# Kernel tuning notes

Hardware: AMD Instinct MI355X
Metric: run time of the kernel (lower is better)

The kernel has to match this reference:

```python
import jax, jax.numpy as jnp
import numpy as np

N_NODES = 50000
N_EDGES = 300000
F_IN, HID, N_CLS = 256, 256, 128


def _glorot_linear(key, fan_in, fan_out):
    # torch.nn.Linear-style uniform init, kaiming bound 1/sqrt(fan_in)
    s = 1.0 / np.sqrt(fan_in)
    return jax.random.uniform(key, (fan_in, fan_out), jnp.float32, -s, s)


def setup_inputs() -> dict:
    key = jax.random.key(0)
    ks = jax.random.split(key, 8)
    x = jax.random.normal(ks[0], (N_NODES, F_IN), jnp.float32)
    edge_index = jax.random.randint(ks[1], (2, N_EDGES), 0, N_NODES, dtype=jnp.int32)
    return {
        "x": x,
        "edge_index": edge_index,
        "W1": _glorot_linear(ks[2], F_IN, HID), "b1": jnp.zeros((HID,), jnp.float32),
        "W2": _glorot_linear(ks[3], HID, HID),  "b2": jnp.zeros((HID,), jnp.float32),
        "W3": _glorot_linear(ks[4], HID, HID),  "b3": jnp.zeros((HID,), jnp.float32),
        "W4": _glorot_linear(ks[5], HID, N_CLS), "b4": jnp.zeros((N_CLS,), jnp.float32),
    }


def _gcn_conv(x, W, b, src, dst, norm, n):
    # x' = D^{-1/2} (A + I) D^{-1/2} X W + b   (PyG GCNConv default)
    h = x @ W                                  # [N, out]
    msg = h[src] * norm[:, None]               # gather + edge scaling  [E', out]
    return jax.ops.segment_sum(msg, dst, num_segments=n) + b


def reference(x, edge_index, W1, b1, W2, b2, W3, b3, W4, b4):
    n = x.shape[0]
    loops = jnp.arange(n, dtype=edge_index.dtype)
    src = jnp.concatenate([edge_index[0], loops])  # add self-loops
    dst = jnp.concatenate([edge_index[1], loops])
    # symmetric normalization: deg over target nodes (unit edge weights)
    deg = jax.ops.segment_sum(jnp.ones_like(dst, jnp.float32), dst, num_segments=n)
    dis = jnp.where(deg > 0, jax.lax.rsqrt(jnp.maximum(deg, 1.0)), 0.0)
    norm = dis[src] * dis[dst]                     # [E']

    h = jax.nn.relu(_gcn_conv(x, W1, b1, src, dst, norm, n))
    h = jax.nn.relu(_gcn_conv(h, W2, b2, src, dst, norm, n))
    h = jax.nn.relu(_gcn_conv(h, W3, b3, src, dst, norm, n))
    h = _gcn_conv(h, W4, b4, src, dst, norm, n)    # [N, C]

    # global_add_pool with batch == zeros -> single-graph sum pool
    pooled = jnp.sum(h, axis=0, keepdims=True)     # [1, C]
    return (pooled, jax.nn.log_softmax(pooled, axis=1))
```

## Files before the change

### kernel.cpp

```cpp
#include <hip/hip_runtime.h>


typedef __attribute__((ext_vector_type(8))) short short8;
typedef __attribute__((ext_vector_type(4))) short short4v;
typedef __attribute__((ext_vector_type(4))) float float4v;

__device__ __forceinline__ unsigned short f2b(float f) {
    unsigned int u = __builtin_bit_cast(unsigned int, f);
    u += 0x7fffu + ((u >> 16) & 1u);
    return (unsigned short)(u >> 16);
}
__device__ __forceinline__ float b2f(unsigned short b) {
    unsigned int u = ((unsigned int)b) << 16;
    return __builtin_bit_cast(float, u);
}


__global__ void count_kernel(const int* __restrict__ dst, int* __restrict__ cnt, int E) {
    int i = blockIdx.x * blockDim.x + threadIdx.x;
    if (i < E) atomicAdd(&cnt[dst[i]], 1);
}

__global__ void blocksum_kernel(const int* __restrict__ cnt, int* __restrict__ bsum, int N) {
    __shared__ int s[256];
    int t = threadIdx.x;
    int i = blockIdx.x * 256 + t;
    s[t] = (i < N) ? cnt[i] : 0;
    __syncthreads();
    for (int d = 128; d > 0; d >>= 1) {
        if (t < d) s[t] += s[t + d];
        __syncthreads();
    }
    if (t == 0) bsum[blockIdx.x] = s[0];
}

__global__ void bscan_kernel(int* __restrict__ bsum, int B) {
    __shared__ int s[256];
    int t = threadIdx.x;
    int v = (t < B) ? bsum[t] : 0;
    s[t] = v;
    __syncthreads();
    for (int d = 1; d < 256; d <<= 1) {
        int x = (t >= d) ? s[t - d] : 0;
        __syncthreads();
        s[t] += x;
        __syncthreads();
    }
    if (t < B) bsum[t] = s[t] - v;
}

__global__ void finalize_kernel(const int* __restrict__ cnt, const int* __restrict__ bsum,
                                int* __restrict__ offs, int* __restrict__ cursor,
                                float* __restrict__ dis, int N, int E) {
    __shared__ int s[256];
    int t = threadIdx.x;
    int i = blockIdx.x * 256 + t;
    int c = (i < N) ? cnt[i] : 0;
    s[t] = c;
    __syncthreads();
    for (int d = 1; d < 256; d <<= 1) {
        int x = (t >= d) ? s[t - d] : 0;
        __syncthreads();
        s[t] += x;
        __syncthreads();
    }
    if (i < N) {
        int ex = bsum[blockIdx.x] + s[t] - c;
        offs[i] = ex;
        cursor[i] = ex;
        dis[i] = rsqrtf((float)(c + 1));
    }
    if (blockIdx.x == 0 && t == 0) offs[N] = E;
}

__global__ void scatter_kernel(const int* __restrict__ src, const int* __restrict__ dst,
                               const float* __restrict__ dis, int* __restrict__ cursor,
                               int* __restrict__ csr_src, float* __restrict__ csr_nrm, int E) {
    int i = blockIdx.x * blockDim.x + threadIdx.x;
    if (i < E) {
        int s = src[i], d = dst[i];
        int pos = atomicAdd(&cursor[d], 1);
        csr_src[pos] = s;
        csr_nrm[pos] = dis[s] * dis[d];
    }
}

__global__ void outsum_kernel(const int* __restrict__ src, const int* __restrict__ dst,
                              const float* __restrict__ dis, float* __restrict__ t, int E) {
    int i = blockIdx.x * blockDim.x + threadIdx.x;
    if (i < E) atomicAdd(&t[src[i]], dis[dst[i]]);
}


__global__ void convert_x_kernel(const float* __restrict__ x, unsigned short* __restrict__ xb,
                                 int total4) {
    int i = blockIdx.x * blockDim.x + threadIdx.x;
    if (i < total4) {
        float4 v = *(const float4*)&x[i * 4];
        ushort4 o;
        o.x = f2b(v.x); o.y = f2b(v.y); o.z = f2b(v.z); o.w = f2b(v.w);
        *(ushort4*)&xb[i * 4] = o;
    }
}

__global__ void convert_wt_kernel(const float* __restrict__ W1, const float* __restrict__ W2,
                                  const float* __restrict__ W3, unsigned short* __restrict__ Wt1,
                                  unsigned short* __restrict__ Wt2, unsigned short* __restrict__ Wt3) {
    const float* W = (blockIdx.y == 0) ? W1 : (blockIdx.y == 1) ? W2 : W3;
    unsigned short* Wt = (blockIdx.y == 0) ? Wt1 : (blockIdx.y == 1) ? Wt2 : Wt3;
    int n = blockIdx.x;
    int k = threadIdx.x;
    Wt[n * 256 + k] = f2b(W[k * 256 + n]);
}

__global__ __launch_bounds__(256, 2) void gemm_bf16_kernel(
        const unsigned short* __restrict__ A, const unsigned short* __restrict__ Wt,
        unsigned short* __restrict__ C, int M) {
    __shared__ unsigned short As[128 * 72];
    __shared__ unsigned short Bs[128 * 72];
    const int tid = threadIdx.x;
    const int lane = tid & 63;
    const int wave = tid >> 6;
    const int l15 = lane & 15;
    const int quad = lane >> 4;
    const int wm = wave & 1;
    const int wn = wave >> 1;
    const int m0 = blockIdx.x * 128;
    const int n0 = blockIdx.y * 128;

    float4v acc[4][4] = {};

    const int srow = tid >> 3;
    const int skof = (tid & 7) * 8;

    for (int kk = 0; kk < 256; kk += 64) {
#pragma unroll
        for (int p = 0; p < 4; p++) {
            int row = p * 32 + srow;
            int gm = m0 + row;
            float4 av = make_float4(0.f, 0.f, 0.f, 0.f);
            if (gm < M) av = *(const float4*)&A[(size_t)gm * 256 + kk + skof];
            *(float4*)&As[row * 72 + skof] = av;
            float4 bv = *(const float4*)&Wt[(size_t)(n0 + row) * 256 + kk + skof];
            *(float4*)&Bs[row * 72 + skof] = bv;
        }
        __syncthreads();
#pragma unroll
        for (int ks = 0; ks < 64; ks += 32) {
            short8 af[4], bf[4];
#pragma unroll
            for (int mi = 0; mi < 4; mi++)
                af[mi] = *(const short8*)&As[(wm * 64 + mi * 16 + l15) * 72 + ks + quad * 8];
#pragma unroll
            for (int nj = 0; nj < 4; nj++)
                bf[nj] = *(const short8*)&Bs[(wn * 64 + nj * 16 + l15) * 72 + ks + quad * 8];
#pragma unroll
            for (int mi = 0; mi < 4; mi++)
#pragma unroll
                for (int nj = 0; nj < 4; nj++)
                    acc[mi][nj] = __builtin_amdgcn_mfma_f32_16x16x32_bf16(
                        af[mi], bf[nj], acc[mi][nj], 0, 0, 0);
        }
        __syncthreads();
    }

#pragma unroll
    for (int mi = 0; mi < 4; mi++) {
#pragma unroll
        for (int r = 0; r < 4; r++) {
            int row = m0 + wm * 64 + mi * 16 + quad * 4 + r;
            if (row < M) {
#pragma unroll
                for (int nj = 0; nj < 4; nj++) {
                    int col = n0 + wn * 64 + nj * 16 + l15;
                    C[(size_t)row * 256 + col] = f2b(acc[mi][nj][r]);
                }
            }
        }
    }
}

template <int RELU>
__global__ __launch_bounds__(256) void agg_bf16_kernel(
        const unsigned short* __restrict__ T, const float* __restrict__ bias,
        const int* __restrict__ offs, const int* __restrict__ csr_src,
        const float* __restrict__ csr_nrm, const float* __restrict__ dis,
        unsigned short* __restrict__ out, int N) {
    int v = blockIdx.x * 4 + (threadIdx.x >> 6);
    if (v >= N) return;
    int lane = threadIdx.x & 63;
    int f4 = lane * 4;
    int beg = offs[v], end = offs[v + 1];
    float dv = dis[v];
    float w = dv * dv;
    short4v hs = *(const short4v*)&T[(size_t)v * 256 + f4];
    float a0 = w * b2f((unsigned short)hs[0]);
    float a1 = w * b2f((unsigned short)hs[1]);
    float a2 = w * b2f((unsigned short)hs[2]);
    float a3 = w * b2f((unsigned short)hs[3]);
    int e = beg;
    for (; e + 4 <= end; e += 4) {
        int s0 = csr_src[e],     s1 = csr_src[e + 1];
        int s2 = csr_src[e + 2], s3 = csr_src[e + 3];
        float n0 = csr_nrm[e],     n1 = csr_nrm[e + 1];
        float n2 = csr_nrm[e + 2], n3 = csr_nrm[e + 3];
        short4v h0 = *(const short4v*)&T[(size_t)s0 * 256 + f4];
        short4v h1 = *(const short4v*)&T[(size_t)s1 * 256 + f4];
        short4v h2 = *(const short4v*)&T[(size_t)s2 * 256 + f4];
        short4v h3 = *(const short4v*)&T[(size_t)s3 * 256 + f4];
        a0 += n0 * b2f((unsigned short)h0[0]) + n1 * b2f((unsigned short)h1[0])
            + n2 * b2f((unsigned short)h2[0]) + n3 * b2f((unsigned short)h3[0]);
        a1 += n0 * b2f((unsigned short)h0[1]) + n1 * b2f((unsigned short)h1[1])
            + n2 * b2f((unsigned short)h2[1]) + n3 * b2f((unsigned short)h3[1]);
        a2 += n0 * b2f((unsigned short)h0[2]) + n1 * b2f((unsigned short)h1[2])
            + n2 * b2f((unsigned short)h2[2]) + n3 * b2f((unsigned short)h3[2]);
        a3 += n0 * b2f((unsigned short)h0[3]) + n1 * b2f((unsigned short)h1[3])
            + n2 * b2f((unsigned short)h2[3]) + n3 * b2f((unsigned short)h3[3]);
    }
    for (; e < end; e++) {
        int s = csr_src[e];
        float nm = csr_nrm[e];
        short4v h = *(const short4v*)&T[(size_t)s * 256 + f4];
        a0 += nm * b2f((unsigned short)h[0]);
        a1 += nm * b2f((unsigned short)h[1]);
        a2 += nm * b2f((unsigned short)h[2]);
        a3 += nm * b2f((unsigned short)h[3]);
    }
    float4 bv = *(const float4*)&bias[f4];
    a0 += bv.x; a1 += bv.y; a2 += bv.z; a3 += bv.w;
    if (RELU) {
        a0 = fmaxf(a0, 0.f); a1 = fmaxf(a1, 0.f);
        a2 = fmaxf(a2, 0.f); a3 = fmaxf(a3, 0.f);
    }
    uint2 o;
    o.x = (unsigned int)f2b(a0) | ((unsigned int)f2b(a1) << 16);
    o.y = (unsigned int)f2b(a2) | ((unsigned int)f2b(a3) << 16);
    *(uint2*)&out[(size_t)v * 256 + f4] = o;
}

__global__ __launch_bounds__(256) void wpool_partial(
        const unsigned short* __restrict__ H, const float* __restrict__ dis,
        const float* __restrict__ tsum, float* __restrict__ partial, int N) {
    int tid = threadIdx.x;
    int f8 = (tid & 31) * 8;
    int rg = tid >> 5;
    float a[8] = {};
    for (int r = blockIdx.x * 8 + rg; r < N; r += gridDim.x * 8) {
        float s = dis[r] * (dis[r] + tsum[r]);
        short8 h = *(const short8*)&H[(size_t)r * 256 + f8];
#pragma unroll
        for (int i = 0; i < 8; i++) a[i] += s * b2f((unsigned short)h[i]);
    }
    __shared__ float red[8 * 256];
#pragma unroll
    for (int i = 0; i < 8; i++) red[rg * 256 + f8 + i] = a[i];
    __syncthreads();
    for (int s = 4; s > 0; s >>= 1) {
        if (rg < s) {
#pragma unroll
            for (int i = 0; i < 8; i++)
                red[rg * 256 + f8 + i] += red[(rg + s) * 256 + f8 + i];
        }
        __syncthreads();
    }
    partial[(size_t)blockIdx.x * 256 + tid] = red[tid];
}

__global__ void wpool_reduce(const float* __restrict__ partial, float* __restrict__ acc) {
    int f = threadIdx.x;
    int p0 = blockIdx.x * 32;
    float a = 0.f;
#pragma unroll
    for (int p = 0; p < 32; p++) a += partial[(size_t)(p0 + p) * 256 + f];
    atomicAdd(&acc[f], a);
}

__global__ void final_kernel(const float* __restrict__ acc, const float* __restrict__ W4,
                             const float* __restrict__ b4, float* __restrict__ out, int N) {
    __shared__ float red[128];
    int c = threadIdx.x;
    float p = (float)N * b4[c];
    for (int k = 0; k < 256; k++) p += acc[k] * W4[k * 128 + c];
    out[c] = p;
    red[c] = p;
    __syncthreads();
    for (int s = 64; s > 0; s >>= 1) {
        if (c < s) red[c] = fmaxf(red[c], red[c + s]);
        __syncthreads();
    }
    float m = red[0];
    __syncthreads();
    red[c] = expf(p - m);
    __syncthreads();
    for (int s = 64; s > 0; s >>= 1) {
        if (c < s) red[c] += red[c + s];
        __syncthreads();
    }
    float lse = m + logf(red[0]);
    out[128 + c] = p - lse;
}

extern "C" void kernel_launch(void* const* d_in, const int* in_sizes, int n_in,
                              void* d_out, int out_size, void* d_ws, size_t ws_size,
                              hipStream_t stream) {
    const float* x  = (const float*)d_in[0];
    const int*   ei = (const int*)d_in[1];
    const float* W1 = (const float*)d_in[2];
    const float* b1 = (const float*)d_in[3];
    const float* W2 = (const float*)d_in[4];
    const float* b2 = (const float*)d_in[5];
    const float* W3 = (const float*)d_in[6];
    const float* b3 = (const float*)d_in[7];
    const float* W4 = (const float*)d_in[8];
    const float* b4 = (const float*)d_in[9];

    const int N = in_sizes[0] / 256;
    const int E = in_sizes[1] / 2;
    const int* src = ei;
    const int* dst = ei + E;

    char* p = (char*)d_ws;
    auto alloc = [&](size_t bytes) {
        char* r = p;
        p += (bytes + 255) & ~(size_t)255;
        return r;
    };
    int*            cnt     = (int*)alloc((size_t)N * 4);
    int*            offs    = (int*)alloc((size_t)(N + 1) * 4);
    int*            cursor  = (int*)alloc((size_t)N * 4);
    float*          dis     = (float*)alloc((size_t)N * 4);
    float*          tsum    = (float*)alloc((size_t)N * 4);
    int*            bsum    = (int*)alloc(1024 * 4);
    int*            csr_src = (int*)alloc((size_t)E * 4);
    float*          csr_nrm = (float*)alloc((size_t)E * 4);
    unsigned short* xb      = (unsigned short*)alloc((size_t)N * 256 * 2);
    unsigned short* Wt1     = (unsigned short*)alloc(256 * 256 * 2);
    unsigned short* Wt2     = (unsigned short*)alloc(256 * 256 * 2);
    unsigned short* Wt3     = (unsigned short*)alloc(256 * 256 * 2);
    unsigned short* T       = (unsigned short*)alloc((size_t)N * 256 * 2);
    unsigned short* Abuf    = (unsigned short*)alloc((size_t)N * 256 * 2);
    float*          partial = (float*)alloc((size_t)1024 * 256 * 4);
    float*          accbuf  = (float*)alloc(256 * 4);

    hipMemsetAsync(cnt, 0, (size_t)N * 4, stream);
    hipMemsetAsync(tsum, 0, (size_t)N * 4, stream);
    hipMemsetAsync(accbuf, 0, 256 * 4, stream);
    int eb = (E + 255) / 256;
    int nb = (N + 255) / 256;
    count_kernel<<<eb, 256, 0, stream>>>(dst, cnt, E);
    blocksum_kernel<<<nb, 256, 0, stream>>>(cnt, bsum, N);
    bscan_kernel<<<1, 256, 0, stream>>>(bsum, nb);
    finalize_kernel<<<nb, 256, 0, stream>>>(cnt, bsum, offs, cursor, dis, N, E);
    scatter_kernel<<<eb, 256, 0, stream>>>(src, dst, dis, cursor, csr_src, csr_nrm, E);
    outsum_kernel<<<eb, 256, 0, stream>>>(src, dst, dis, tsum, E);

    int total4 = N * 64;
    convert_x_kernel<<<(total4 + 255) / 256, 256, 0, stream>>>(x, xb, total4);
    convert_wt_kernel<<<dim3(256, 3), 256, 0, stream>>>(W1, W2, W3, Wt1, Wt2, Wt3);

    dim3 ggrid((N + 127) / 128, 2);
    int ab = (N + 3) / 4;
    gemm_bf16_kernel<<<ggrid, 256, 0, stream>>>(xb, Wt1, T, N);
    agg_bf16_kernel<1><<<ab, 256, 0, stream>>>(T, b1, offs, csr_src, csr_nrm, dis, Abuf, N);
    gemm_bf16_kernel<<<ggrid, 256, 0, stream>>>(Abuf, Wt2, T, N);
    agg_bf16_kernel<1><<<ab, 256, 0, stream>>>(T, b2, offs, csr_src, csr_nrm, dis, Abuf, N);
    gemm_bf16_kernel<<<ggrid, 256, 0, stream>>>(Abuf, Wt3, T, N);
    agg_bf16_kernel<1><<<ab, 256, 0, stream>>>(T, b3, offs, csr_src, csr_nrm, dis, Abuf, N);

    wpool_partial<<<1024, 256, 0, stream>>>(Abuf, dis, tsum, partial, N);
    wpool_reduce<<<32, 256, 0, stream>>>(partial, accbuf);
    final_kernel<<<1, 128, 0, stream>>>(accbuf, W4, b4, (float*)d_out, N);
}
```

Baseline: 361.3 us.

## Fuse fp32-to-bf16 input conversion into first GEMM and merge preprocessing kernels

Removes the separate pass that converts x to bf16: the first GEMM now reads fp32 x directly and converts while filling shared memory. The scatter and out-degree-sum kernels are merged into one pass over the edges, and three memsets become a single zero kernel. GEMM launch bounds go from 2 to 3 blocks per unit. This cuts launches and a full N x 256 round trip through memory, in exchange for the first GEMM reading twice the bytes per tile (though the two column-split blocks each read x) and possible register pressure from the higher occupancy bound.

```diff
diff --git a/kernel.cpp b/kernel.cpp
--- a/kernel.cpp
+++ b/kernel.cpp
@@ -15,6 +15,13 @@
     return __builtin_bit_cast(float, u);
 }
 
+
+__global__ void zero_kernel(int* __restrict__ cnt, float* __restrict__ tsum,
+                            float* __restrict__ acc, int N) {
+    int i = blockIdx.x * 256 + threadIdx.x;
+    if (i < N) { cnt[i] = 0; tsum[i] = 0.f; }
+    if (i < 256) acc[i] = 0.f;
+}
 
 __global__ void count_kernel(const int* __restrict__ dst, int* __restrict__ cnt, int E) {
     int i = blockIdx.x * blockDim.x + threadIdx.x;
@@ -73,35 +80,21 @@
     if (blockIdx.x == 0 && t == 0) offs[N] = E;
 }
 
-__global__ void scatter_kernel(const int* __restrict__ src, const int* __restrict__ dst,
-                               const float* __restrict__ dis, int* __restrict__ cursor,
-                               int* __restrict__ csr_src, float* __restrict__ csr_nrm, int E) {
+__global__ void scatter_outsum_kernel(const int* __restrict__ src, const int* __restrict__ dst,
+                                      const float* __restrict__ dis, int* __restrict__ cursor,
+                                      int* __restrict__ csr_src, float* __restrict__ csr_nrm,
+                                      float* __restrict__ tsum, int E) {
     int i = blockIdx.x * blockDim.x + threadIdx.x;
     if (i < E) {
         int s = src[i], d = dst[i];
+        float dd = dis[d];
         int pos = atomicAdd(&cursor[d], 1);
         csr_src[pos] = s;
-        csr_nrm[pos] = dis[s] * dis[d];
-    }
-}
-
-__global__ void outsum_kernel(const int* __restrict__ src, const int* __restrict__ dst,
-                              const float* __restrict__ dis, float* __restrict__ t, int E) {
-    int i = blockIdx.x * blockDim.x + threadIdx.x;
-    if (i < E) atomicAdd(&t[src[i]], dis[dst[i]]);
-}
-
-
-__global__ void convert_x_kernel(const float* __restrict__ x, unsigned short* __restrict__ xb,
-                                 int total4) {
-    int i = blockIdx.x * blockDim.x + threadIdx.x;
-    if (i < total4) {
-        float4 v = *(const float4*)&x[i * 4];
-        ushort4 o;
-        o.x = f2b(v.x); o.y = f2b(v.y); o.z = f2b(v.z); o.w = f2b(v.w);
-        *(ushort4*)&xb[i * 4] = o;
-    }
-}
+        csr_nrm[pos] = dis[s] * dd;
+        atomicAdd(&tsum[s], dd);
+    }
+}
+
 
 __global__ void convert_wt_kernel(const float* __restrict__ W1, const float* __restrict__ W2,
                                   const float* __restrict__ W3, unsigned short* __restrict__ Wt1,
@@ -113,8 +106,9 @@
     Wt[n * 256 + k] = f2b(W[k * 256 + n]);
 }
 
-__global__ __launch_bounds__(256, 2) void gemm_bf16_kernel(
-        const unsigned short* __restrict__ A, const unsigned short* __restrict__ Wt,
+template <int AFP32>
+__global__ __launch_bounds__(256, 3) void gemm_bf16_kernel(
+        const void* __restrict__ Ap, const unsigned short* __restrict__ Wt,
         unsigned short* __restrict__ C, int M) {
     __shared__ unsigned short As[128 * 72];
     __shared__ unsigned short Bs[128 * 72];
@@ -138,9 +132,26 @@
         for (int p = 0; p < 4; p++) {
             int row = p * 32 + srow;
             int gm = m0 + row;
-            float4 av = make_float4(0.f, 0.f, 0.f, 0.f);
-            if (gm < M) av = *(const float4*)&A[(size_t)gm * 256 + kk + skof];
-            *(float4*)&As[row * 72 + skof] = av;
+            if (AFP32) {
+                const float* Af = (const float*)Ap;
+                float4 lo = make_float4(0.f, 0.f, 0.f, 0.f);
+                float4 hi = make_float4(0.f, 0.f, 0.f, 0.f);
+                if (gm < M) {
+                    lo = *(const float4*)&Af[(size_t)gm * 256 + kk + skof];
+                    hi = *(const float4*)&Af[(size_t)gm * 256 + kk + skof + 4];
+                }
+                union { unsigned short u[8]; float4 v; } pk;
+                pk.u[0] = f2b(lo.x); pk.u[1] = f2b(lo.y);
+                pk.u[2] = f2b(lo.z); pk.u[3] = f2b(lo.w);
+                pk.u[4] = f2b(hi.x); pk.u[5] = f2b(hi.y);
+                pk.u[6] = f2b(hi.z); pk.u[7] = f2b(hi.w);
+                *(float4*)&As[row * 72 + skof] = pk.v;
+            } else {
+                const unsigned short* Ab = (const unsigned short*)Ap;
+                float4 av = make_float4(0.f, 0.f, 0.f, 0.f);
+                if (gm < M) av = *(const float4*)&Ab[(size_t)gm * 256 + kk + skof];
+                *(float4*)&As[row * 72 + skof] = av;
+            }
             float4 bv = *(const float4*)&Wt[(size_t)(n0 + row) * 256 + kk + skof];
             *(float4*)&Bs[row * 72 + skof] = bv;
         }
@@ -333,7 +344,6 @@
     int*            bsum    = (int*)alloc(1024 * 4);
     int*            csr_src = (int*)alloc((size_t)E * 4);
     float*          csr_nrm = (float*)alloc((size_t)E * 4);
-    unsigned short* xb      = (unsigned short*)alloc((size_t)N * 256 * 2);
     unsigned short* Wt1     = (unsigned short*)alloc(256 * 256 * 2);
     unsigned short* Wt2     = (unsigned short*)alloc(256 * 256 * 2);
     unsigned short* Wt3     = (unsigned short*)alloc(256 * 256 * 2);
@@ -342,29 +352,25 @@
     float*          partial = (float*)alloc((size_t)1024 * 256 * 4);
     float*          accbuf  = (float*)alloc(256 * 4);
 
-    hipMemsetAsync(cnt, 0, (size_t)N * 4, stream);
-    hipMemsetAsync(tsum, 0, (size_t)N * 4, stream);
-    hipMemsetAsync(accbuf, 0, 256 * 4, stream);
     int eb = (E + 255) / 256;
     int nb = (N + 255) / 256;
+    zero_kernel<<<nb, 256, 0, stream>>>(cnt, tsum, accbuf, N);
     count_kernel<<<eb, 256, 0, stream>>>(dst, cnt, E);
     blocksum_kernel<<<nb, 256, 0, stream>>>(cnt, bsum, N);
     bscan_kernel<<<1, 256, 0, stream>>>(bsum, nb);
     finalize_kernel<<<nb, 256, 0, stream>>>(cnt, bsum, offs, cursor, dis, N, E);
-    scatter_kernel<<<eb, 256, 0, stream>>>(src, dst, dis, cursor, csr_src, csr_nrm, E);
-    outsum_kernel<<<eb, 256, 0, stream>>>(src, dst, dis, tsum, E);
-
-    int total4 = N * 64;
-    convert_x_kernel<<<(total4 + 255) / 256, 256, 0, stream>>>(x, xb, total4);
+    scatter_outsum_kernel<<<eb, 256, 0, stream>>>(src, dst, dis, cursor, csr_src,
+                                                  csr_nrm, tsum, E);
+
     convert_wt_kernel<<<dim3(256, 3), 256, 0, stream>>>(W1, W2, W3, Wt1, Wt2, Wt3);
 
     dim3 ggrid((N + 127) / 128, 2);
     int ab = (N + 3) / 4;
-    gemm_bf16_kernel<<<ggrid, 256, 0, stream>>>(xb, Wt1, T, N);
+    gemm_bf16_kernel<1><<<ggrid, 256, 0, stream>>>(x, Wt1, T, N);
     agg_bf16_kernel<1><<<ab, 256, 0, stream>>>(T, b1, offs, csr_src, csr_nrm, dis, Abuf, N);
-    gemm_bf16_kernel<<<ggrid, 256, 0, stream>>>(Abuf, Wt2, T, N);
+    gemm_bf16_kernel<0><<<ggrid, 256, 0, stream>>>(Abuf, Wt2, T, N);
     agg_bf16_kernel<1><<<ab, 256, 0, stream>>>(T, b2, offs, csr_src, csr_nrm, dis, Abuf, N);
-    gemm_bf16_kernel<<<ggrid, 256, 0, stream>>>(Abuf, Wt3, T, N);
+    gemm_bf16_kernel<0><<<ggrid, 256, 0, stream>>>(Abuf, Wt3, T, N);
     agg_bf16_kernel<1><<<ab, 256, 0, stream>>>(T, b3, offs, csr_src, csr_nrm, dis, Abuf, N);
 
     wpool_partial<<<1024, 256, 0, stream>>>(Abuf, dis, tsum, partial, N);
```

After: 343.3 us. -5.0%, faster.
